# Performance work log

Measured on AMD Instinct MI355X. Metric: run time of the kernel, lower is better.

## Reference

```python
import jax, jax.numpy as jnp
import numpy as np

C_Z = 128
C_H = 128
EPS = 1e-5


def _layer_norm(x, g, b):
    mu = jnp.mean(x, axis=-1, keepdims=True)
    var = jnp.var(x, axis=-1, keepdims=True)
    return (x - mu) * jax.lax.rsqrt(var + EPS) * g + b


def setup_inputs() -> dict:
    key = jax.random.key(0)
    ks = jax.random.split(key, 8)
    B, N = 1, 512
    z = jax.random.normal(ks[0], (B, N, N, C_Z), dtype=jnp.float32)
    mask = jnp.ones((B, N, N), dtype=jnp.float32)
    s = 0.02
    return {
        "z": z,
        "mask": mask,
        "ln_in_g": jnp.ones((C_Z,), jnp.float32),
        "ln_in_b": jnp.zeros((C_Z,), jnp.float32),
        "w_ap": jax.random.normal(ks[1], (C_Z, C_H), jnp.float32) * s,
        "b_ap": jnp.zeros((C_H,), jnp.float32),
        "w_ag": jax.random.normal(ks[2], (C_Z, C_H), jnp.float32) * s,
        "b_ag": jnp.zeros((C_H,), jnp.float32),
        "w_bp": jax.random.normal(ks[3], (C_Z, C_H), jnp.float32) * s,
        "b_bp": jnp.zeros((C_H,), jnp.float32),
        "w_bg": jax.random.normal(ks[4], (C_Z, C_H), jnp.float32) * s,
        "b_bg": jnp.zeros((C_H,), jnp.float32),
        "w_g": jax.random.normal(ks[5], (C_Z, C_Z), jnp.float32) * s,
        "b_g": jnp.zeros((C_Z,), jnp.float32),
        "ln_out_g": jnp.ones((C_H,), jnp.float32),
        "ln_out_b": jnp.zeros((C_H,), jnp.float32),
        "w_z": jax.random.normal(ks[6], (C_H, C_Z), jnp.float32) * s,
        "b_z": jnp.zeros((C_Z,), jnp.float32),
    }


def reference(z, mask, ln_in_g, ln_in_b, w_ap, b_ap, w_ag, b_ag,
              w_bp, b_bp, w_bg, b_bg, w_g, b_g, ln_out_g, ln_out_b, w_z, b_z):
    m = mask[..., None]                                  # [B,N,N,1]
    zn = _layer_norm(z, ln_in_g, ln_in_b)                # [B,N,N,Cz]
    a = m * jax.nn.sigmoid(zn @ w_ag + b_ag) * (zn @ w_ap + b_ap)  # [B,N,N,H]
    b = m * jax.nn.sigmoid(zn @ w_bg + b_bg) * (zn @ w_bp + b_bp)  # [B,N,N,H]
    # outgoing triangle: x[i,k] = sum_j a[i,j] * b[k,j]  (per hidden channel)
    x = jnp.einsum("bijh,bkjh->bikh", a, b)
    x = _layer_norm(x, ln_out_g, ln_out_b) @ w_z + b_z   # [B,N,N,Cz]
    g = jax.nn.sigmoid(zn @ w_g + b_g)
    return x * g
```

## Files before the change

### kernel.cpp

```cpp
#include <hip/hip_runtime.h>
#include <stdint.h>

#define NPOS 262144
#define EPS_LN 1e-5f
#define ZSTRIDE 272

typedef _Float16 f16x8_t __attribute__((ext_vector_type(8)));
typedef float f32x4_t __attribute__((ext_vector_type(4)));

static __device__ __forceinline__ unsigned short f2h(float f) {
    union { _Float16 h; unsigned short u; } v;
    v.h = (_Float16)f;
    return v.u;
}
static __device__ __forceinline__ float h2f(unsigned short u) {
    union { unsigned short u; _Float16 h; } v;
    v.u = u;
    return (float)v.h;
}
static __device__ __forceinline__ float sigmoidf_(float x) {
    return 1.0f / (1.0f + __expf(-x));
}

#define GLOAD_LDS16(gp, lp) __builtin_amdgcn_global_load_lds( \
    (const __attribute__((address_space(1))) void*)(gp), \
    (__attribute__((address_space(3))) void*)(lp), 16, 0, 0)

__global__ __launch_bounds__(256)
void k_prep6(const float* w0, const float* w1, const float* w2,
             const float* w3, const float* w4, const float* w5,
             const float* lng, const float* lnog, unsigned short* wt) {
    const float* srcs[6] = {w0, w1, w2, w3, w4, w5};
    const float* src = srcs[blockIdx.x];
    const float* fold = (blockIdx.x == 4) ? lnog : lng;
    unsigned short* dst = wt + blockIdx.x * 16384;
    for (int rep = 0; rep < 64; ++rep) {
        int idx = rep * 256 + threadIdx.x;
        int h = idx >> 7, k = idx & 127;
        dst[idx] = f2h(src[k * 128 + h] * fold[k]);
    }
}

__global__ __launch_bounds__(128)
void k_const(const float* wap, const float* wag, const float* wbp,
             const float* wbg, const float* wz, const float* wg,
             const float* lng, const float* lnb,
             const float* lnog, const float* lnob, float* cc) {
    const float* Ws[6] = {wap, wag, wbp, wbg, wz, wg};
    const float* W = Ws[blockIdx.x];
    const float* gv = (blockIdx.x == 4) ? lnog : lng;
    const float* bv = (blockIdx.x == 4) ? lnob : lnb;
    int c = threadIdx.x;
    float s1 = 0.f, s2 = 0.f;
    for (int k = 0; k < 128; ++k) {
        float wv = W[k * 128 + c];
        s1 += gv[k] * wv;
        s2 += bv[k] * wv;
    }
    cc[blockIdx.x * 256 + c] = s1;
    cc[blockIdx.x * 256 + 128 + c] = s2;
}

__global__ __launch_bounds__(256)
void k1h(const float* __restrict__ z, const float* __restrict__ mask,
         const unsigned short* __restrict__ wt, const float* __restrict__ cc,
         const float* __restrict__ b_ap, const float* __restrict__ b_ag,
         const float* __restrict__ b_bp, const float* __restrict__ b_bg,
         unsigned short* __restrict__ a_t, unsigned short* __restrict__ b_t,
         unsigned short* __restrict__ z16, unsigned* __restrict__ mustd)
{
    __shared__ char sZ[64 * ZSTRIDE];
    __shared__ float smu[64];
    __shared__ float srstd[64];
    const int t = threadIdx.x;
    const int lane = t & 63;
    const int w = t >> 6;
    const int g = lane >> 4;
    const int l15 = lane & 15;
    const int p0 = blockIdx.x * 64;

    {
        const int pos = t >> 2, q = t & 3;
        const float* zp = z + (size_t)(p0 + pos) * 128 + q * 32;
        float s = 0.f, s2 = 0.f;
        #pragma unroll
        for (int e = 0; e < 8; ++e) {
            float4 v = *(const float4*)(zp + e * 4);
            s += v.x + v.y + v.z + v.w;
            s2 += v.x * v.x + v.y * v.y + v.z * v.z + v.w * v.w;
            uint2 st;
            st.x = f2h(v.x) | ((unsigned)f2h(v.y) << 16);
            st.y = f2h(v.z) | ((unsigned)f2h(v.w) << 16);
            *(uint2*)(sZ + pos * ZSTRIDE + (q * 32 + e * 4) * 2) = st;
            *(uint2*)(z16 + (size_t)(p0 + pos) * 128 + q * 32 + e * 4) = st;
        }
        s  += __shfl_xor(s, 1);  s  += __shfl_xor(s, 2);
        s2 += __shfl_xor(s2, 1); s2 += __shfl_xor(s2, 2);
        float mu = s * (1.0f / 128.0f);
        float var = s2 * (1.0f / 128.0f) - mu * mu;
        float rstd = rsqrtf(var + EPS_LN);
        if (q == 0) {
            smu[pos] = mu;
            srstd[pos] = rstd;
            mustd[p0 + pos] = f2h(mu) | ((unsigned)f2h(rstd) << 16);
        }
    }
    __syncthreads();

    const size_t blkBase = (size_t)(blockIdx.x >> 1) * 16384;
    const int pq = (blockIdx.x & 1) * 64;

    #pragma unroll 1
    for (int hp = 0; hp < 2; ++hp) {
        const int h = hp * 64 + w * 16 + l15;
        f16x8_t wapf[4], wagf[4], wbpf[4], wbgf[4];
        #pragma unroll
        for (int kk = 0; kk < 4; ++kk) {
            int off = h * 128 + kk * 32 + g * 8;
            wapf[kk] = *(const f16x8_t*)(wt + 0 * 16384 + off);
            wagf[kk] = *(const f16x8_t*)(wt + 1 * 16384 + off);
            wbpf[kk] = *(const f16x8_t*)(wt + 2 * 16384 + off);
            wbgf[kk] = *(const f16x8_t*)(wt + 3 * 16384 + off);
        }
        const float C1ap = cc[0 * 256 + h], C2ap = cc[0 * 256 + 128 + h];
        const float C1ag = cc[1 * 256 + h], C2ag = cc[1 * 256 + 128 + h];
        const float C1bp = cc[2 * 256 + h], C2bp = cc[2 * 256 + 128 + h];
        const float C1bg = cc[3 * 256 + h], C2bg = cc[3 * 256 + 128 + h];
        const float bap = b_ap[h], bag = b_ag[h];
        const float bbp = b_bp[h], bbg = b_bg[h];

        unsigned short* aBlk = a_t + blkBase + (size_t)h * 128 + pq;
        unsigned short* bBlk = b_t + blkBase + (size_t)h * 128 + pq;

        f32x4_t zero = {0.f, 0.f, 0.f, 0.f};
        for (int rt = 0; rt < 4; ++rt) {
            f32x4_t accAP = zero, accAG = zero, accBP = zero, accBG = zero;
            #pragma unroll
            for (int kk = 0; kk < 4; ++kk) {
                f16x8_t ax = *(const f16x8_t*)(sZ + (rt * 16 + l15) * ZSTRIDE + kk * 64 + g * 16);
                accAP = __builtin_amdgcn_mfma_f32_16x16x32_f16(ax, wapf[kk], accAP, 0, 0, 0);
                accAG = __builtin_amdgcn_mfma_f32_16x16x32_f16(ax, wagf[kk], accAG, 0, 0, 0);
                accBP = __builtin_amdgcn_mfma_f32_16x16x32_f16(ax, wbpf[kk], accBP, 0, 0, 0);
                accBG = __builtin_amdgcn_mfma_f32_16x16x32_f16(ax, wbgf[kk], accBG, 0, 0, 0);
            }
            int lp = rt * 16 + g * 4;
            int pb = p0 + lp;
            unsigned short pka[4], pkb[4];
            #pragma unroll
            for (int r = 0; r < 4; ++r) {
                float mu = smu[lp + r];
                float rstd = srstd[lp + r];
                float vAP = rstd * (accAP[r] - mu * C1ap) + C2ap + bap;
                float vAG = rstd * (accAG[r] - mu * C1ag) + C2ag + bag;
                float vBP = rstd * (accBP[r] - mu * C1bp) + C2bp + bbp;
                float vBG = rstd * (accBG[r] - mu * C1bg) + C2bg + bbg;
                float m = mask[pb + r];
                pka[r] = f2h(m * sigmoidf_(vAG) * vAP);
                pkb[r] = f2h(m * sigmoidf_(vBG) * vBP);
            }
            uint2 sta, stb;
            sta.x = pka[0] | ((unsigned)pka[1] << 16);
            sta.y = pka[2] | ((unsigned)pka[3] << 16);
            stb.x = pkb[0] | ((unsigned)pkb[1] << 16);
            stb.y = pkb[2] | ((unsigned)pkb[3] << 16);
            *(uint2*)(aBlk + lp) = sta;
            *(uint2*)(bBlk + lp) = stb;
        }
    }
}

__global__ __launch_bounds__(256, 2)
void k2_tri(const unsigned short* __restrict__ a_t,
            const unsigned short* __restrict__ b_t,
            unsigned short* __restrict__ x_t) {
    __shared__ char sA[16384];
    __shared__ char sB[16384];
    const int t = threadIdx.x;
    const int lane = t & 63;
    const int w = t >> 6;
    const int wr = w >> 1, wc = w & 1;
    const int h = blockIdx.y;
    const int i0 = (blockIdx.x >> 2) * 128;
    const int k0 = (blockIdx.x & 3) * 128;
    const int kb4 = (blockIdx.x & 3);
    const size_t hoff = (size_t)h * 128;

    f32x4_t zero = {0.f, 0.f, 0.f, 0.f};
    f32x4_t acc[4][4];
    #pragma unroll
    for (int m = 0; m < 4; ++m)
        #pragma unroll
        for (int n = 0; n < 4; ++n) acc[m][n] = zero;

    for (int kt = 0; kt < 8; ++kt) {
        const int kb = (kt >> 1), ko = (kt & 1) * 64;
        #pragma unroll
        for (int pass = 0; pass < 4; ++pass) {
            int ci = pass * 256 + t;
            int row = ci >> 3, ch = ci & 7;
            const unsigned short* gA = a_t +
                (size_t)((i0 + row) * 4 + kb) * 16384 + hoff + ko + ch * 8;
            const unsigned short* gB = b_t +
                (size_t)((k0 + row) * 4 + kb) * 16384 + hoff + ko + ch * 8;
            GLOAD_LDS16(gA, sA + w * 1024 + pass * 4096);
            GLOAD_LDS16(gB, sB + w * 1024 + pass * 4096);
        }
        __syncthreads();
        #pragma unroll
        for (int ks = 0; ks < 2; ++ks) {
            f16x8_t af[4], bf[4];
            #pragma unroll
            for (int m = 0; m < 4; ++m) {
                int ar = wr * 64 + m * 16 + (lane & 15);
                af[m] = *(const f16x8_t*)(sA + ar * 128 + ks * 64 + (lane >> 4) * 16);
            }
            #pragma unroll
            for (int n = 0; n < 4; ++n) {
                int br = wc * 64 + n * 16 + (lane & 15);
                bf[n] = *(const f16x8_t*)(sB + br * 128 + ks * 64 + (lane >> 4) * 16);
            }
            #pragma unroll
            for (int m = 0; m < 4; ++m)
                #pragma unroll
                for (int n = 0; n < 4; ++n)
                    acc[m][n] = __builtin_amdgcn_mfma_f32_16x16x32_f16(af[m], bf[n], acc[m][n], 0, 0, 0);
        }
        __syncthreads();
    }
    #pragma unroll
    for (int m = 0; m < 4; ++m) {
        int ibase = i0 + wr * 64 + m * 16 + (lane >> 4) * 4;
        #pragma unroll
        for (int n = 0; n < 4; ++n) {
            int ppos = wc * 64 + n * 16 + (lane & 15);
            #pragma unroll
            for (int r = 0; r < 4; ++r) {
                x_t[(size_t)((ibase + r) * 4 + kb4) * 16384 + hoff + ppos] =
                    f2h(acc[m][n][r]);
            }
        }
    }
}

__global__ __launch_bounds__(512, 2)
void k3d(const unsigned short* __restrict__ x_t,
         const unsigned short* __restrict__ z16,
         const unsigned* __restrict__ mustd,
         const unsigned short* __restrict__ wt, const float* __restrict__ cc,
         const float* __restrict__ b_z, const float* __restrict__ b_g,
         float* __restrict__ out)
{
    __shared__ char sX[128 * ZSTRIDE];
    __shared__ float smuX[128], srstdX[128];
    __shared__ float smuZ[128], srstdZ[128];
    const int t = threadIdx.x, lane = t & 63, w = t >> 6;
    const int g = lane >> 4;
    const int c = w * 16 + (lane & 15);
    const int p0 = blockIdx.x * 128;

    f16x8_t wzf[4], wgf[4];
    #pragma unroll
    for (int kk = 0; kk < 4; ++kk) {
        int off = c * 128 + kk * 32 + g * 8;
        wzf[kk] = *(const f16x8_t*)(wt + 4 * 16384 + off);
        wgf[kk] = *(const f16x8_t*)(wt + 5 * 16384 + off);
    }
    const float bzv = b_z[c], bgv = b_g[c];
    const float C1z = cc[4 * 256 + c], C2z = cc[4 * 256 + 128 + c];
    const float C1g = cc[5 * 256 + c], C2g = cc[5 * 256 + 128 + c];

    if (t < 128) {
        unsigned v = mustd[p0 + t];
        smuZ[t] = h2f((unsigned short)(v & 0xffffu));
        srstdZ[t] = h2f((unsigned short)(v >> 16));
    }

    {
        const unsigned short* xb = x_t + (size_t)blockIdx.x * 16384;
        const int hp = lane;
        const int ps = w * 16;
        const unsigned short* x0 = xb + (2 * hp) * 128 + ps;
        const unsigned short* x1 = xb + (2 * hp + 1) * 128 + ps;
        uint4 a0 = *(const uint4*)(x0);
        uint4 a1 = *(const uint4*)(x0 + 8);
        uint4 b0 = *(const uint4*)(x1);
        uint4 b1 = *(const uint4*)(x1 + 8);
        unsigned aw[8] = {a0.x, a0.y, a0.z, a0.w, a1.x, a1.y, a1.z, a1.w};
        unsigned bw[8] = {b0.x, b0.y, b0.z, b0.w, b1.x, b1.y, b1.z, b1.w};
        #pragma unroll
        for (int e = 0; e < 8; ++e) {
            int p = ps + 2 * e;
            *(unsigned*)(sX + p * ZSTRIDE + hp * 4) =
                (aw[e] & 0xffffu) | ((bw[e] & 0xffffu) << 16);
            *(unsigned*)(sX + (p + 1) * ZSTRIDE + hp * 4) =
                (aw[e] >> 16) | ((bw[e] >> 16) << 16);
        }
    }
    __syncthreads();
    {
        int pos = t >> 2, q = t & 3;
        float s = 0.f, s2 = 0.f;
        #pragma unroll
        for (int e = 0; e < 8; ++e) {
            uint2 vv = *(const uint2*)(sX + pos * ZSTRIDE + (q * 32 + e * 4) * 2);
            float v0 = h2f((unsigned short)(vv.x & 0xffffu));
            float v1 = h2f((unsigned short)(vv.x >> 16));
            float v2 = h2f((unsigned short)(vv.y & 0xffffu));
            float v3 = h2f((unsigned short)(vv.y >> 16));
            s  += v0 + v1 + v2 + v3;
            s2 += v0 * v0 + v1 * v1 + v2 * v2 + v3 * v3;
        }
        s  += __shfl_xor(s, 1);  s  += __shfl_xor(s, 2);
        s2 += __shfl_xor(s2, 1); s2 += __shfl_xor(s2, 2);
        float mu = s * (1.0f / 128.0f);
        float var = s2 * (1.0f / 128.0f) - mu * mu;
        if (q == 0) {
            smuX[pos] = mu;
            srstdX[pos] = rsqrtf(var + EPS_LN);
        }
    }
    __syncthreads();
    f32x4_t zero = {0.f, 0.f, 0.f, 0.f};
    for (int rt = 0; rt < 8; ++rt) {
        f32x4_t accX = zero, accG = zero;
        #pragma unroll
        for (int kk = 0; kk < 4; ++kk) {
            int row = rt * 16 + (lane & 15);
            f16x8_t ax = *(const f16x8_t*)(sX + row * ZSTRIDE + kk * 64 + g * 16);
            f16x8_t az = *(const f16x8_t*)(z16 + (size_t)(p0 + row) * 128 + kk * 32 + g * 8);
            accX = __builtin_amdgcn_mfma_f32_16x16x32_f16(ax, wzf[kk], accX, 0, 0, 0);
            accG = __builtin_amdgcn_mfma_f32_16x16x32_f16(az, wgf[kk], accG, 0, 0, 0);
        }
        int lr0 = rt * 16 + g * 4;
        #pragma unroll
        for (int r = 0; r < 4; ++r) {
            int lr = lr0 + r;
            float oz = srstdX[lr] * (accX[r] - smuX[lr] * C1z) + C2z + bzv;
            float lg = srstdZ[lr] * (accG[r] - smuZ[lr] * C1g) + C2g + bgv;
            out[(size_t)(p0 + lr) * 128 + c] = oz * sigmoidf_(lg);
        }
    }
}

extern "C" void kernel_launch(void* const* d_in, const int* in_sizes, int n_in,
                              void* d_out, int out_size, void* d_ws, size_t ws_size,
                              hipStream_t stream) {
    const float* z        = (const float*)d_in[0];
    const float* mask     = (const float*)d_in[1];
    const float* ln_in_g  = (const float*)d_in[2];
    const float* ln_in_b  = (const float*)d_in[3];
    const float* w_ap     = (const float*)d_in[4];
    const float* b_ap     = (const float*)d_in[5];
    const float* w_ag     = (const float*)d_in[6];
    const float* b_ag     = (const float*)d_in[7];
    const float* w_bp     = (const float*)d_in[8];
    const float* b_bp     = (const float*)d_in[9];
    const float* w_bg     = (const float*)d_in[10];
    const float* b_bg     = (const float*)d_in[11];
    const float* w_g      = (const float*)d_in[12];
    const float* b_g      = (const float*)d_in[13];
    const float* ln_out_g = (const float*)d_in[14];
    const float* ln_out_b = (const float*)d_in[15];
    const float* w_z      = (const float*)d_in[16];
    const float* b_z      = (const float*)d_in[17];
    float* out = (float*)d_out;

    char* ws = (char*)d_ws;
    const size_t MB64 = (size_t)NPOS * 128 * 2;
    unsigned short* wt   = (unsigned short*)(ws);
    float*          cc   = (float*)(ws + 786432);
    unsigned*      mustd = (unsigned*)(ws + (1 << 20));
    unsigned short* a_t  = (unsigned short*)(ws + (2 << 20));
    unsigned short* b_t  = (unsigned short*)(ws + (2 << 20) + MB64);
    unsigned short* x_t  = (unsigned short*)(ws + (2 << 20) + 2 * MB64);
    unsigned short* z16  = (unsigned short*)(ws + (2 << 20) + 3 * MB64);

    k_prep6<<<6, 256, 0, stream>>>(w_ap, w_ag, w_bp, w_bg, w_z, w_g,
                                   ln_in_g, ln_out_g, wt);
    k_const<<<6, 128, 0, stream>>>(w_ap, w_ag, w_bp, w_bg, w_z, w_g,
                                   ln_in_g, ln_in_b, ln_out_g, ln_out_b, cc);
    k1h<<<4096, 256, 0, stream>>>(z, mask, wt, cc,
                                  b_ap, b_ag, b_bp, b_bg,
                                  a_t, b_t, z16, mustd);
    k2_tri<<<dim3(16, 128), 256, 0, stream>>>(a_t, b_t, x_t);
    k3d<<<2048, 512, 0, stream>>>(x_t, z16, mustd, wt, cc, b_z, b_g, out);
}
```

Baseline: 336.2 us.

## Double-buffer LDS tiles in triangle GEMM to overlap loads with MFMA

The triangle-multiply kernel now keeps two LDS buffers for A and B. It issues the global-to-LDS loads for the next k-tile before running the MFMA work on the current tile, so memory latency overlaps with compute. This doubles shared memory per block to 64KB, which may reduce occupancy from the requested 2 blocks per CU. Only one barrier per iteration remains, and the code relies on it to order the async LDS loads, which is a correctness risk if the loads are not waited on.

```diff
diff --git a/kernel.cpp b/kernel.cpp
--- a/kernel.cpp
+++ b/kernel.cpp
@@ -173,8 +173,8 @@
 void k2_tri(const unsigned short* __restrict__ a_t,
             const unsigned short* __restrict__ b_t,
             unsigned short* __restrict__ x_t) {
-    __shared__ char sA[16384];
-    __shared__ char sB[16384];
+    __shared__ char sA[2][16384];
+    __shared__ char sB[2][16384];
     const int t = threadIdx.x;
     const int lane = t & 63;
     const int w = t >> 6;
@@ -184,6 +184,7 @@
     const int k0 = (blockIdx.x & 3) * 128;
     const int kb4 = (blockIdx.x & 3);
     const size_t hoff = (size_t)h * 128;
+    const int srow = t >> 3, sch = t & 7;
 
     f32x4_t zero = {0.f, 0.f, 0.f, 0.f};
     f32x4_t acc[4][4];
@@ -192,32 +193,49 @@
         #pragma unroll
         for (int n = 0; n < 4; ++n) acc[m][n] = zero;
 
+    {
+        const int kb = 0, ko = 0;
+        #pragma unroll
+        for (int pass = 0; pass < 4; ++pass) {
+            int row = pass * 32 + srow;
+            const unsigned short* gA = a_t +
+                (size_t)((i0 + row) * 4 + kb) * 16384 + hoff + ko + sch * 8;
+            const unsigned short* gB = b_t +
+                (size_t)((k0 + row) * 4 + kb) * 16384 + hoff + ko + sch * 8;
+            GLOAD_LDS16(gA, sA[0] + w * 1024 + pass * 4096);
+            GLOAD_LDS16(gB, sB[0] + w * 1024 + pass * 4096);
+        }
+    }
+    __syncthreads();
+
+    int cur = 0;
     for (int kt = 0; kt < 8; ++kt) {
-        const int kb = (kt >> 1), ko = (kt & 1) * 64;
-        #pragma unroll
-        for (int pass = 0; pass < 4; ++pass) {
-            int ci = pass * 256 + t;
-            int row = ci >> 3, ch = ci & 7;
-            const unsigned short* gA = a_t +
-                (size_t)((i0 + row) * 4 + kb) * 16384 + hoff + ko + ch * 8;
-            const unsigned short* gB = b_t +
-                (size_t)((k0 + row) * 4 + kb) * 16384 + hoff + ko + ch * 8;
-            GLOAD_LDS16(gA, sA + w * 1024 + pass * 4096);
-            GLOAD_LDS16(gB, sB + w * 1024 + pass * 4096);
-        }
-        __syncthreads();
+        if (kt < 7) {
+            const int ktn = kt + 1;
+            const int kb = (ktn >> 1), ko = (ktn & 1) * 64;
+            #pragma unroll
+            for (int pass = 0; pass < 4; ++pass) {
+                int row = pass * 32 + srow;
+                const unsigned short* gA = a_t +
+                    (size_t)((i0 + row) * 4 + kb) * 16384 + hoff + ko + sch * 8;
+                const unsigned short* gB = b_t +
+                    (size_t)((k0 + row) * 4 + kb) * 16384 + hoff + ko + sch * 8;
+                GLOAD_LDS16(gA, sA[cur ^ 1] + w * 1024 + pass * 4096);
+                GLOAD_LDS16(gB, sB[cur ^ 1] + w * 1024 + pass * 4096);
+            }
+        }
         #pragma unroll
         for (int ks = 0; ks < 2; ++ks) {
             f16x8_t af[4], bf[4];
             #pragma unroll
             for (int m = 0; m < 4; ++m) {
                 int ar = wr * 64 + m * 16 + (lane & 15);
-                af[m] = *(const f16x8_t*)(sA + ar * 128 + ks * 64 + (lane >> 4) * 16);
+                af[m] = *(const f16x8_t*)(sA[cur] + ar * 128 + ks * 64 + (lane >> 4) * 16);
             }
             #pragma unroll
             for (int n = 0; n < 4; ++n) {
                 int br = wc * 64 + n * 16 + (lane & 15);
-                bf[n] = *(const f16x8_t*)(sB + br * 128 + ks * 64 + (lane >> 4) * 16);
+                bf[n] = *(const f16x8_t*)(sB[cur] + br * 128 + ks * 64 + (lane >> 4) * 16);
             }
             #pragma unroll
             for (int m = 0; m < 4; ++m)
@@ -226,7 +244,9 @@
                     acc[m][n] = __builtin_amdgcn_mfma_f32_16x16x32_f16(af[m], bf[n], acc[m][n], 0, 0, 0);
         }
         __syncthreads();
-    }
+        cur ^= 1;
+    }
+
     #pragma unroll
     for (int m = 0; m < 4; ++m) {
         int ibase = i0 + wr * 64 + m * 16 + (lane >> 4) * 4;
```

New measurement: 338.7 us. About the same (+0.7%).
